# Performance work log

Hardware: AMD Instinct MI355X
Metric: run time of the kernel (lower is better)

The kernel has to match this reference:

```python
import jax, jax.numpy as jnp
import numpy as np

N_NODES = 50000
N_EDGES = 800000
IN_C, HID, OUT_C, T = 64, 64, 64, 16


def setup_inputs() -> dict:
    key = jax.random.key(0)
    ks = jax.random.split(key, 9)
    x = jax.random.normal(ks[0], (N_NODES, IN_C, T), dtype=jnp.float32)
    edge_index = jax.random.randint(ks[1], (2, N_EDGES), 0, N_NODES, dtype=jnp.int32)
    edge_attr = jax.random.uniform(ks[2], (N_EDGES, T), dtype=jnp.float32)
    s1 = 1.0 / np.sqrt(IN_C)
    s2 = 1.0 / np.sqrt(HID)
    s3 = 1.0 / np.sqrt(OUT_C)
    W1 = jax.random.uniform(ks[3], (IN_C, HID), jnp.float32, -s1, s1)
    b1 = jnp.zeros((HID,), jnp.float32)
    W2 = jax.random.uniform(ks[4], (HID, OUT_C), jnp.float32, -s2, s2)
    b2 = jnp.zeros((OUT_C,), jnp.float32)
    Wout = jax.random.uniform(ks[5], (OUT_C, OUT_C), jnp.float32, -s3, s3)
    bout = jax.random.uniform(ks[6], (OUT_C,), jnp.float32, -s3, s3)
    return {"x": x, "edge_index": edge_index, "edge_attr": edge_attr,
            "W1": W1, "b1": b1, "W2": W2, "b2": b2, "Wout": Wout, "bout": bout}


def _gcn_conv(h, src, dst, ew, W, b, n_nodes):
    # h: [N, d_in] -> [N, d_out]; GCNConv with edge weights + self-loops,
    # symmetric normalization D^-1/2 A D^-1/2, aggregation at dst (col).
    h = h @ W
    deg = jax.ops.segment_sum(ew, dst, num_segments=n_nodes) + 1.0  # self-loop weight 1
    dinv = jnp.where(deg > 0, deg ** -0.5, 0.0)
    norm = dinv[src] * ew * dinv[dst]                       # [E]
    agg = jax.ops.segment_sum(h[src] * norm[:, None], dst, num_segments=n_nodes)
    agg = agg + h * (dinv * dinv)[:, None]                  # self-loop message
    return agg + b


def reference(x, edge_index, edge_attr, W1, b1, W2, b2, Wout, bout):
    n_nodes = x.shape[0]
    xa = x.mean(axis=-1)                # temporal mean aggregation: [N, in_c]
    ew = edge_attr[:, -1]               # last-step edge weight: [E]
    src, dst = edge_index[0], edge_index[1]
    h = _gcn_conv(xa, src, dst, ew, W1, b1, n_nodes)
    h = jax.nn.relu(h)
    h = _gcn_conv(h, src, dst, ew, W2, b2, n_nodes)
    return h @ Wout + bout              # output head, Identity activation
```

## Files before the change

kernel.cpp:

```cpp
#include <hip/hip_runtime.h>

#define CAP 64
#define OVF_MAX 8192


__device__ __forceinline__ void stage_W(const float* __restrict__ W,
                                        float4* __restrict__ Wt, int tid) {
    int l = tid & 63, qq = tid >> 6;
    #pragma unroll
    for (int s = 0; s < 4; ++s) {
        int q = qq * 4 + s;
        float4 v = make_float4(W[(4 * q + 0) * 64 + l],
                               W[(4 * q + 1) * 64 + l],
                               W[(4 * q + 2) * 64 + l],
                               W[(4 * q + 3) * 64 + l]);
        Wt[q * 64 + l] = v;
    }
}


__global__ void k_pre(int* __restrict__ cur, int* __restrict__ ovfc, int N,
                      const float* __restrict__ W2, const float* __restrict__ Wout,
                      const float* __restrict__ b2, const float* __restrict__ bout,
                      float* __restrict__ Wc, float* __restrict__ bc, int zb) {
    int tid = threadIdx.x;
    int bid = blockIdx.x;
    if (bid < zb) {
        int i = bid * 256 + tid;
        if (i < N) cur[i] = 0;
        if (i == N) *ovfc = 0;
        return;
    }
    int wb = bid - zb;
    if (wb < 16) {
        int idx = wb * 256 + tid;
        int j = idx >> 6, i = idx & 63;
        float s = 0.0f;
        #pragma unroll 8
        for (int m = 0; m < 64; ++m)
            s = fmaf(W2[i * 64 + m], Wout[m * 64 + j], s);
        Wc[i * 64 + j] = s;
    } else if (tid < 64) {
        float s = bout[tid];
        for (int k = 0; k < 64; ++k)
            s = fmaf(b2[k], Wout[k * 64 + tid], s);
        bc[tid] = s;
    }
}

__global__ __launch_bounds__(256) void k_scatmean(
        const int* __restrict__ ei, const float* __restrict__ ea,
        int* __restrict__ cur, int2* __restrict__ eb,
        int* __restrict__ ovf_cnt, int4* __restrict__ ovf,
        int E, int scatterBlocks,
        const float* __restrict__ x, const float* __restrict__ W1,
        float* __restrict__ h1, int N, int meanBlocks) {
    int tid = threadIdx.x;
    int bid = (int)blockIdx.x;
    int nmin = scatterBlocks < meanBlocks ? scatterBlocks : meanBlocks;
    int isScat, rid;
    if (bid < 2 * nmin) { isScat = !(bid & 1); rid = bid >> 1; }
    else { isScat = (scatterBlocks > meanBlocks); rid = bid - 2 * nmin + nmin; }

    if (isScat) {
        int e = rid * 256 + tid;
        if (e < E) {
            int s = ei[e];
            int d = ei[E + e];
            float w = ea[(size_t)e * 16 + 15];
            int p = atomicAdd(cur + d, 1);
            if (p < CAP) {
                eb[(size_t)d * CAP + p] = make_int2(s, __float_as_int(w));
            } else {
                int q = atomicAdd(ovf_cnt, 1);
                if (q < OVF_MAX) ovf[q] = make_int4(s, d, __float_as_int(w), 0);
            }
        }
        return;
    }
    __shared__ float4 Wt[16 * 64];
    __shared__ float rbuf[4 * 64];
    stage_W(W1, Wt, tid);
    __syncthreads();
    int w = tid >> 6, l = tid & 63;
    float* rw = rbuf + w * 64;
    for (int it = 0; it < 4; ++it) {
        int n = rid * 16 + it * 4 + w;
        if (n >= N) continue;
        const float4* xp = (const float4*)(x + (size_t)n * 1024);
        float4 v0 = xp[l], v1 = xp[64 + l], v2 = xp[128 + l], v3 = xp[192 + l];
        float s0 = (v0.x + v0.y) + (v0.z + v0.w);
        float s1 = (v1.x + v1.y) + (v1.z + v1.w);
        float s2 = (v2.x + v2.y) + (v2.z + v2.w);
        float s3 = (v3.x + v3.y) + (v3.z + v3.w);
        s0 += __shfl_xor(s0, 1); s0 += __shfl_xor(s0, 2);
        s1 += __shfl_xor(s1, 1); s1 += __shfl_xor(s1, 2);
        s2 += __shfl_xor(s2, 1); s2 += __shfl_xor(s2, 2);
        s3 += __shfl_xor(s3, 1); s3 += __shfl_xor(s3, 2);
        if ((l & 3) == 0) {
            int q = l >> 2;
            rw[q]      = s0 * 0.0625f;
            rw[q + 16] = s1 * 0.0625f;
            rw[q + 32] = s2 * 0.0625f;
            rw[q + 48] = s3 * 0.0625f;
        }
        float acc = 0.0f;
        const float4* rb4 = (const float4*)rw;
        #pragma unroll
        for (int q = 0; q < 16; ++q) {
            float4 rv = rb4[q];
            float4 wv = Wt[q * 64 + l];
            acc = fmaf(rv.x, wv.x, acc);
            acc = fmaf(rv.y, wv.y, acc);
            acc = fmaf(rv.z, wv.z, acc);
            acc = fmaf(rv.w, wv.w, acc);
        }
        h1[(size_t)n * 64 + l] = acc;
    }
}

__global__ void k_dinvb(const int* __restrict__ cur, const int2* __restrict__ eb,
                        const int* __restrict__ ovf_cnt, const int4* __restrict__ ovf,
                        float* __restrict__ dinv, int N) {
    int tid = threadIdx.x;
    int n = blockIdx.x * 64 + (tid >> 2);
    int j = tid & 3;
    if (n >= N) return;
    int mfull = cur[n];
    int m = mfull > CAP ? CAP : mfull;
    float s = 0.0f;
    for (int i = j; i < m; i += 4) s += __int_as_float(eb[(size_t)n * CAP + i].y);
    s += __shfl_xor(s, 1);
    s += __shfl_xor(s, 2);
    if (j == 0) {
        if (mfull > CAP) {
            int oc = *ovf_cnt; if (oc > OVF_MAX) oc = OVF_MAX;
            for (int k = 0; k < oc; ++k) {
                int4 o = ovf[k];
                if (o.y == n) s += __int_as_float(o.z);
            }
        }
        dinv[n] = 1.0f / sqrtf(s + 1.0f);
    }
}

__global__ __launch_bounds__(256) void k_agg1(const float* __restrict__ in,
                                              const float* __restrict__ bias,
                                              const float* __restrict__ dinv,
                                              const int* __restrict__ cur,
                                              const int2* __restrict__ eb,
                                              const int* __restrict__ ovf_cnt,
                                              const int4* __restrict__ ovf,
                                              float* __restrict__ out, int N) {
    int tid = threadIdx.x;
    int w = tid >> 6, c = tid & 63;
    float bias_c = bias[c];
    for (int it = 0; it < 4; ++it) {
        int n = blockIdx.x * 16 + it * 4 + w;
        if (n >= N) continue;
        float dv = dinv[n];
        float selfv = in[(size_t)n * 64 + c];
        float a0 = 0.f, a1 = 0.f, a2 = 0.f, a3 = 0.f;
        const int2* bkt = eb + (size_t)n * CAP;
        int mfull = cur[n];
        int m = mfull > CAP ? CAP : mfull;
        int i = 0;
        for (; i + 8 <= m; i += 8) {
            int2 e0 = bkt[i + 0], e1 = bkt[i + 1], e2 = bkt[i + 2], e3 = bkt[i + 3];
            int2 e4 = bkt[i + 4], e5 = bkt[i + 5], e6 = bkt[i + 6], e7 = bkt[i + 7];
            float d0 = dinv[e0.x], d1 = dinv[e1.x], d2 = dinv[e2.x], d3 = dinv[e3.x];
            float d4 = dinv[e4.x], d5 = dinv[e5.x], d6 = dinv[e6.x], d7 = dinv[e7.x];
            float v0 = in[(size_t)e0.x * 64 + c], v1 = in[(size_t)e1.x * 64 + c];
            float v2 = in[(size_t)e2.x * 64 + c], v3 = in[(size_t)e3.x * 64 + c];
            float v4 = in[(size_t)e4.x * 64 + c], v5 = in[(size_t)e5.x * 64 + c];
            float v6 = in[(size_t)e6.x * 64 + c], v7 = in[(size_t)e7.x * 64 + c];
            a0 = fmaf(v0, __int_as_float(e0.y) * d0, a0);
            a1 = fmaf(v1, __int_as_float(e1.y) * d1, a1);
            a2 = fmaf(v2, __int_as_float(e2.y) * d2, a2);
            a3 = fmaf(v3, __int_as_float(e3.y) * d3, a3);
            a0 = fmaf(v4, __int_as_float(e4.y) * d4, a0);
            a1 = fmaf(v5, __int_as_float(e5.y) * d5, a1);
            a2 = fmaf(v6, __int_as_float(e6.y) * d6, a2);
            a3 = fmaf(v7, __int_as_float(e7.y) * d7, a3);
        }
        for (; i < m; ++i) {
            int2 e = bkt[i];
            a0 = fmaf(in[(size_t)e.x * 64 + c], __int_as_float(e.y) * dinv[e.x], a0);
        }
        if (mfull > CAP) {
            int oc = *ovf_cnt; if (oc > OVF_MAX) oc = OVF_MAX;
            for (int k = 0; k < oc; ++k) {
                int4 o = ovf[k];
                if (o.y == n)
                    a0 = fmaf(in[(size_t)o.x * 64 + c], __int_as_float(o.z) * dinv[o.x], a0);
            }
        }
        float r = fmaf(dv, ((a0 + a1) + (a2 + a3)) + selfv * dv, bias_c);
        out[(size_t)n * 64 + c] = fmaxf(r, 0.0f);
    }
}

__global__ __launch_bounds__(256) void k_agg2(const float* __restrict__ in,
                                              const float* __restrict__ Wc,
                                              const float* __restrict__ bc,
                                              const float* __restrict__ dinv,
                                              const int* __restrict__ cur,
                                              const int2* __restrict__ eb,
                                              const int* __restrict__ ovf_cnt,
                                              const int4* __restrict__ ovf,
                                              float* __restrict__ out, int N) {
    __shared__ float4 Wt[16 * 64];
    __shared__ float rbuf[4 * 64];
    int tid = threadIdx.x;
    stage_W(Wc, Wt, tid);
    __syncthreads();
    int w = tid >> 6, c = tid & 63;
    float bc_c = bc[c];
    float* rw = rbuf + w * 64;
    for (int it = 0; it < 4; ++it) {
        int n = blockIdx.x * 16 + it * 4 + w;
        if (n >= N) continue;
        float dv = dinv[n];
        float selfv = in[(size_t)n * 64 + c];
        float a0 = 0.f, a1 = 0.f, a2 = 0.f, a3 = 0.f;
        const int2* bkt = eb + (size_t)n * CAP;
        int mfull = cur[n];
        int m = mfull > CAP ? CAP : mfull;
        int i = 0;
        for (; i + 8 <= m; i += 8) {
            int2 e0 = bkt[i + 0], e1 = bkt[i + 1], e2 = bkt[i + 2], e3 = bkt[i + 3];
            int2 e4 = bkt[i + 4], e5 = bkt[i + 5], e6 = bkt[i + 6], e7 = bkt[i + 7];
            float d0 = dinv[e0.x], d1 = dinv[e1.x], d2 = dinv[e2.x], d3 = dinv[e3.x];
            float d4 = dinv[e4.x], d5 = dinv[e5.x], d6 = dinv[e6.x], d7 = dinv[e7.x];
            float v0 = in[(size_t)e0.x * 64 + c], v1 = in[(size_t)e1.x * 64 + c];
            float v2 = in[(size_t)e2.x * 64 + c], v3 = in[(size_t)e3.x * 64 + c];
            float v4 = in[(size_t)e4.x * 64 + c], v5 = in[(size_t)e5.x * 64 + c];
            float v6 = in[(size_t)e6.x * 64 + c], v7 = in[(size_t)e7.x * 64 + c];
            a0 = fmaf(v0, __int_as_float(e0.y) * d0, a0);
            a1 = fmaf(v1, __int_as_float(e1.y) * d1, a1);
            a2 = fmaf(v2, __int_as_float(e2.y) * d2, a2);
            a3 = fmaf(v3, __int_as_float(e3.y) * d3, a3);
            a0 = fmaf(v4, __int_as_float(e4.y) * d4, a0);
            a1 = fmaf(v5, __int_as_float(e5.y) * d5, a1);
            a2 = fmaf(v6, __int_as_float(e6.y) * d6, a2);
            a3 = fmaf(v7, __int_as_float(e7.y) * d7, a3);
        }
        for (; i < m; ++i) {
            int2 e = bkt[i];
            a0 = fmaf(in[(size_t)e.x * 64 + c], __int_as_float(e.y) * dinv[e.x], a0);
        }
        if (mfull > CAP) {
            int oc = *ovf_cnt; if (oc > OVF_MAX) oc = OVF_MAX;
            for (int k = 0; k < oc; ++k) {
                int4 o = ovf[k];
                if (o.y == n)
                    a0 = fmaf(in[(size_t)o.x * 64 + c], __int_as_float(o.z) * dinv[o.x], a0);
            }
        }
        float r = dv * (((a0 + a1) + (a2 + a3)) + selfv * dv);
        rw[c] = r;
        float acc = bc_c;
        const float4* rb4 = (const float4*)rw;
        #pragma unroll
        for (int q = 0; q < 16; ++q) {
            float4 rv = rb4[q];
            float4 wv = Wt[q * 64 + c];
            acc = fmaf(rv.x, wv.x, acc);
            acc = fmaf(rv.y, wv.y, acc);
            acc = fmaf(rv.z, wv.z, acc);
            acc = fmaf(rv.w, wv.w, acc);
        }
        out[(size_t)n * 64 + c] = acc;
    }
}


extern "C" void kernel_launch(void* const* d_in, const int* in_sizes, int n_in,
                              void* d_out, int out_size, void* d_ws, size_t ws_size,
                              hipStream_t stream) {
    const float* x    = (const float*)d_in[0];
    const int*   ei   = (const int*)d_in[1];
    const float* ea   = (const float*)d_in[2];
    const float* W1   = (const float*)d_in[3];
    const float* b1   = (const float*)d_in[4];
    const float* W2   = (const float*)d_in[5];
    const float* b2   = (const float*)d_in[6];
    const float* Wout = (const float*)d_in[7];
    const float* bout = (const float*)d_in[8];
    float* out = (float*)d_out;

    const int N = in_sizes[0] / (64 * 16);
    const int E = in_sizes[1] / 2;

    char* wsb = (char*)d_ws;
    int4*  ovf  = (int4*)wsb;
    int2*  eb   = (int2*)(wsb + OVF_MAX * 16);
    float* H1   = (float*)(wsb + OVF_MAX * 16 + (size_t)N * CAP * 8);
    size_t NC = (size_t)N * 64;
    float* Z    = H1 + NC;
    int*   cur  = (int*)(Z + NC);
    float* dinv = (float*)(cur + N);
    int*   ovfc = (int*)(dinv + N);
    float* Wc   = (float*)(ovfc + 4);
    float* bc   = Wc + 4096;

    dim3 b256(256);
    int meanBlocks    = (N + 15) / 16;
    int scatterBlocks = (E + 255) / 256;
    int zb = (N + 256) / 256;

    hipLaunchKernelGGL(k_pre, dim3(zb + 17), b256, 0, stream,
                       cur, ovfc, N, W2, Wout, b2, bout, Wc, bc, zb);
    hipLaunchKernelGGL(k_scatmean, dim3(scatterBlocks + meanBlocks), b256, 0, stream,
                       ei, ea, cur, eb, ovfc, ovf, E, scatterBlocks, x, W1, H1, N, meanBlocks);
    hipLaunchKernelGGL(k_dinvb, dim3((N + 63) / 64), b256, 0, stream,
                       cur, eb, ovfc, ovf, dinv, N);
    hipLaunchKernelGGL(k_agg1, dim3(meanBlocks), b256, 0, stream,
                       H1, b1, dinv, cur, eb, ovfc, ovf, Z, N);
    hipLaunchKernelGGL(k_agg2, dim3(meanBlocks), b256, 0, stream,
                       Z, Wc, bc, dinv, cur, eb, ovfc, ovf, out, N);
}
```

Measured before the change: 185.9 us.

## Split per-destination edge buckets into four partitions to reduce atomic contention

After: 224.2 us. +20.6%, slower.

```diff
diff --git a/kernel.cpp b/kernel.cpp
--- a/kernel.cpp
+++ b/kernel.cpp
@@ -1,6 +1,7 @@
 #include <hip/hip_runtime.h>
 
-#define CAP 64
+#define NPART 4
+#define CAP_P 16
 #define OVF_MAX 8192
 
 
@@ -27,8 +28,8 @@
     int bid = blockIdx.x;
     if (bid < zb) {
         int i = bid * 256 + tid;
-        if (i < N) cur[i] = 0;
-        if (i == N) *ovfc = 0;
+        if (i < NPART * N) cur[i] = 0;
+        if (i == NPART * N) *ovfc = 0;
         return;
     }
     int wb = bid - zb;
@@ -63,17 +64,22 @@
     else { isScat = (scatterBlocks > meanBlocks); rid = bid - 2 * nmin + nmin; }
 
     if (isScat) {
-        int e = rid * 256 + tid;
-        if (e < E) {
-            int s = ei[e];
-            int d = ei[E + e];
-            float w = ea[(size_t)e * 16 + 15];
-            int p = atomicAdd(cur + d, 1);
-            if (p < CAP) {
-                eb[(size_t)d * CAP + p] = make_int2(s, __float_as_int(w));
-            } else {
-                int q = atomicAdd(ovf_cnt, 1);
-                if (q < OVF_MAX) ovf[q] = make_int4(s, d, __float_as_int(w), 0);
+        #pragma unroll
+        for (int h = 0; h < 2; ++h) {
+            int e = rid * 512 + h * 256 + tid;
+            if (e < E) {
+                int s = ei[e];
+                int d = ei[E + e];
+                float w = ea[(size_t)e * 16 + 15];
+                int part = e & 3;
+                int p = atomicAdd(cur + part * N + d, 1);
+                if (p < CAP_P) {
+                    eb[((size_t)d * NPART + part) * CAP_P + p] =
+                        make_int2(s, __float_as_int(w));
+                } else {
+                    int q = atomicAdd(ovf_cnt, 1);
+                    if (q < OVF_MAX) ovf[q] = make_int4(s, d, __float_as_int(w), 0);
+                }
             }
         }
         return;
@@ -126,14 +132,16 @@
     int n = blockIdx.x * 64 + (tid >> 2);
     int j = tid & 3;
     if (n >= N) return;
-    int mfull = cur[n];
-    int m = mfull > CAP ? CAP : mfull;
+    int mfull = cur[j * N + n];
+    int m = mfull > CAP_P ? CAP_P : mfull;
+    const int2* b = eb + ((size_t)n * NPART + j) * CAP_P;
     float s = 0.0f;
-    for (int i = j; i < m; i += 4) s += __int_as_float(eb[(size_t)n * CAP + i].y);
-    s += __shfl_xor(s, 1);
-    s += __shfl_xor(s, 2);
+    for (int i = 0; i < m; ++i) s += __int_as_float(b[i].y);
+    int ov = (mfull > CAP_P) ? 1 : 0;
+    s += __shfl_xor(s, 1); ov += __shfl_xor(ov, 1);
+    s += __shfl_xor(s, 2); ov += __shfl_xor(ov, 2);
     if (j == 0) {
-        if (mfull > CAP) {
+        if (ov) {
             int oc = *ovf_cnt; if (oc > OVF_MAX) oc = OVF_MAX;
             for (int k = 0; k < oc; ++k) {
                 int4 o = ovf[k];
@@ -143,6 +151,45 @@
         dinv[n] = 1.0f / sqrtf(s + 1.0f);
     }
 }
+
+#define GATHER_BODY(in_, n_, c_, a0, a1, a2, a3, anyovf)                         \
+    {                                                                            \
+        for (int part = 0; part < NPART; ++part) {                               \
+            int mf = cur[part * N + (n_)];                                       \
+            int m = mf > CAP_P ? CAP_P : mf;                                     \
+            anyovf |= (mf > CAP_P);                                              \
+            const int2* bkt = eb + ((size_t)(n_) * NPART + part) * CAP_P;        \
+            int i = 0;                                                           \
+            for (; i + 4 <= m; i += 4) {                                         \
+                int2 e0 = bkt[i + 0], e1 = bkt[i + 1];                           \
+                int2 e2 = bkt[i + 2], e3 = bkt[i + 3];                           \
+                float d0 = dinv[e0.x], d1 = dinv[e1.x];                          \
+                float d2 = dinv[e2.x], d3 = dinv[e3.x];                          \
+                float v0 = in_[(size_t)e0.x * 64 + (c_)];                        \
+                float v1 = in_[(size_t)e1.x * 64 + (c_)];                        \
+                float v2 = in_[(size_t)e2.x * 64 + (c_)];                        \
+                float v3 = in_[(size_t)e3.x * 64 + (c_)];                        \
+                a0 = fmaf(v0, __int_as_float(e0.y) * d0, a0);                    \
+                a1 = fmaf(v1, __int_as_float(e1.y) * d1, a1);                    \
+                a2 = fmaf(v2, __int_as_float(e2.y) * d2, a2);                    \
+                a3 = fmaf(v3, __int_as_float(e3.y) * d3, a3);                    \
+            }                                                                    \
+            for (; i < m; ++i) {                                                 \
+                int2 e = bkt[i];                                                 \
+                a0 = fmaf(in_[(size_t)e.x * 64 + (c_)],                          \
+                          __int_as_float(e.y) * dinv[e.x], a0);                  \
+            }                                                                    \
+        }                                                                        \
+        if (anyovf) {                                                            \
+            int oc = *ovf_cnt; if (oc > OVF_MAX) oc = OVF_MAX;                   \
+            for (int k = 0; k < oc; ++k) {                                       \
+                int4 o = ovf[k];                                                 \
+                if (o.y == (n_))                                                 \
+                    a0 = fmaf(in_[(size_t)o.x * 64 + (c_)],                      \
+                              __int_as_float(o.z) * dinv[o.x], a0);              \
+            }                                                                    \
+        }                                                                        \
+    }
 
 __global__ __launch_bounds__(256) void k_agg1(const float* __restrict__ in,
                                               const float* __restrict__ bias,
@@ -161,40 +208,8 @@
         float dv = dinv[n];
         float selfv = in[(size_t)n * 64 + c];
         float a0 = 0.f, a1 = 0.f, a2 = 0.f, a3 = 0.f;
-        const int2* bkt = eb + (size_t)n * CAP;
-        int mfull = cur[n];
-        int m = mfull > CAP ? CAP : mfull;
-        int i = 0;
-        for (; i + 8 <= m; i += 8) {
-            int2 e0 = bkt[i + 0], e1 = bkt[i + 1], e2 = bkt[i + 2], e3 = bkt[i + 3];
-            int2 e4 = bkt[i + 4], e5 = bkt[i + 5], e6 = bkt[i + 6], e7 = bkt[i + 7];
-            float d0 = dinv[e0.x], d1 = dinv[e1.x], d2 = dinv[e2.x], d3 = dinv[e3.x];
-            float d4 = dinv[e4.x], d5 = dinv[e5.x], d6 = dinv[e6.x], d7 = dinv[e7.x];
-            float v0 = in[(size_t)e0.x * 64 + c], v1 = in[(size_t)e1.x * 64 + c];
-            float v2 = in[(size_t)e2.x * 64 + c], v3 = in[(size_t)e3.x * 64 + c];
-            float v4 = in[(size_t)e4.x * 64 + c], v5 = in[(size_t)e5.x * 64 + c];
-            float v6 = in[(size_t)e6.x * 64 + c], v7 = in[(size_t)e7.x * 64 + c];
-            a0 = fmaf(v0, __int_as_float(e0.y) * d0, a0);
-            a1 = fmaf(v1, __int_as_float(e1.y) * d1, a1);
-            a2 = fmaf(v2, __int_as_float(e2.y) * d2, a2);
-            a3 = fmaf(v3, __int_as_float(e3.y) * d3, a3);
-            a0 = fmaf(v4, __int_as_float(e4.y) * d4, a0);
-            a1 = fmaf(v5, __int_as_float(e5.y) * d5, a1);
-            a2 = fmaf(v6, __int_as_float(e6.y) * d6, a2);
-            a3 = fmaf(v7, __int_as_float(e7.y) * d7, a3);
-        }
-        for (; i < m; ++i) {
-            int2 e = bkt[i];
-            a0 = fmaf(in[(size_t)e.x * 64 + c], __int_as_float(e.y) * dinv[e.x], a0);
-        }
-        if (mfull > CAP) {
-            int oc = *ovf_cnt; if (oc > OVF_MAX) oc = OVF_MAX;
-            for (int k = 0; k < oc; ++k) {
-                int4 o = ovf[k];
-                if (o.y == n)
-                    a0 = fmaf(in[(size_t)o.x * 64 + c], __int_as_float(o.z) * dinv[o.x], a0);
-            }
-        }
+        int anyovf = 0;
+        GATHER_BODY(in, n, c, a0, a1, a2, a3, anyovf)
         float r = fmaf(dv, ((a0 + a1) + (a2 + a3)) + selfv * dv, bias_c);
         out[(size_t)n * 64 + c] = fmaxf(r, 0.0f);
     }
@@ -223,40 +238,8 @@
         float dv = dinv[n];
         float selfv = in[(size_t)n * 64 + c];
         float a0 = 0.f, a1 = 0.f, a2 = 0.f, a3 = 0.f;
-        const int2* bkt = eb + (size_t)n * CAP;
-        int mfull = cur[n];
-        int m = mfull > CAP ? CAP : mfull;
-        int i = 0;
-        for (; i + 8 <= m; i += 8) {
-            int2 e0 = bkt[i + 0], e1 = bkt[i + 1], e2 = bkt[i + 2], e3 = bkt[i + 3];
-            int2 e4 = bkt[i + 4], e5 = bkt[i + 5], e6 = bkt[i + 6], e7 = bkt[i + 7];
-            float d0 = dinv[e0.x], d1 = dinv[e1.x], d2 = dinv[e2.x], d3 = dinv[e3.x];
-            float d4 = dinv[e4.x], d5 = dinv[e5.x], d6 = dinv[e6.x], d7 = dinv[e7.x];
-            float v0 = in[(size_t)e0.x * 64 + c], v1 = in[(size_t)e1.x * 64 + c];
-            float v2 = in[(size_t)e2.x * 64 + c], v3 = in[(size_t)e3.x * 64 + c];
-            float v4 = in[(size_t)e4.x * 64 + c], v5 = in[(size_t)e5.x * 64 + c];
-            float v6 = in[(size_t)e6.x * 64 + c], v7 = in[(size_t)e7.x * 64 + c];
-            a0 = fmaf(v0, __int_as_float(e0.y) * d0, a0);
-            a1 = fmaf(v1, __int_as_float(e1.y) * d1, a1);
-            a2 = fmaf(v2, __int_as_float(e2.y) * d2, a2);
-            a3 = fmaf(v3, __int_as_float(e3.y) * d3, a3);
-            a0 = fmaf(v4, __int_as_float(e4.y) * d4, a0);
-            a1 = fmaf(v5, __int_as_float(e5.y) * d5, a1);
-            a2 = fmaf(v6, __int_as_float(e6.y) * d6, a2);
-            a3 = fmaf(v7, __int_as_float(e7.y) * d7, a3);
-        }
-        for (; i < m; ++i) {
-            int2 e = bkt[i];
-            a0 = fmaf(in[(size_t)e.x * 64 + c], __int_as_float(e.y) * dinv[e.x], a0);
-        }
-        if (mfull > CAP) {
-            int oc = *ovf_cnt; if (oc > OVF_MAX) oc = OVF_MAX;
-            for (int k = 0; k < oc; ++k) {
-                int4 o = ovf[k];
-                if (o.y == n)
-                    a0 = fmaf(in[(size_t)o.x * 64 + c], __int_as_float(o.z) * dinv[o.x], a0);
-            }
-        }
+        int anyovf = 0;
+        GATHER_BODY(in, n, c, a0, a1, a2, a3, anyovf)
         float r = dv * (((a0 + a1) + (a2 + a3)) + selfv * dv);
         rw[c] = r;
         float acc = bc_c;
@@ -295,19 +278,19 @@
     char* wsb = (char*)d_ws;
     int4*  ovf  = (int4*)wsb;
     int2*  eb   = (int2*)(wsb + OVF_MAX * 16);
-    float* H1   = (float*)(wsb + OVF_MAX * 16 + (size_t)N * CAP * 8);
+    float* H1   = (float*)(wsb + OVF_MAX * 16 + (size_t)N * NPART * CAP_P * 8);
     size_t NC = (size_t)N * 64;
     float* Z    = H1 + NC;
     int*   cur  = (int*)(Z + NC);
-    float* dinv = (float*)(cur + N);
+    float* dinv = (float*)(cur + (size_t)NPART * N);
     int*   ovfc = (int*)(dinv + N);
     float* Wc   = (float*)(ovfc + 4);
     float* bc   = Wc + 4096;
 
     dim3 b256(256);
     int meanBlocks    = (N + 15) / 16;
-    int scatterBlocks = (E + 255) / 256;
-    int zb = (N + 256) / 256;
+    int scatterBlocks = (E + 511) / 512;
+    int zb = (NPART * N + 256) / 256;
 
     hipLaunchKernelGGL(k_pre, dim3(zb + 17), b256, 0, stream,
                        cur, ovfc, N, W2, Wout, b2, bout, Wc, bc, zb);
```
